# Performance work log

Hardware: AMD Instinct MI355X
Metric: run time of the kernel (lower is better)

## Reference

```python
import jax, jax.numpy as jnp
import numpy as np

H = 8  # num_heads


def setup_inputs() -> dict:
    key = jax.random.key(0)
    ks = jax.random.split(key, 10)
    B, N, C_sp, C_fd = 16, 4096, 768, 512
    s = 0.02
    return {
        "spatial_tokens": jax.random.normal(ks[0], (B, N, C_sp), jnp.float32),
        "freq_token": jax.random.normal(ks[1], (B, C_fd), jnp.float32),
        "Wq": jax.random.normal(ks[2], (C_sp, C_sp), jnp.float32) * s,
        "bq": jax.random.normal(ks[3], (C_sp,), jnp.float32) * s,
        "Wk": jax.random.normal(ks[4], (C_sp, C_fd), jnp.float32) * s,
        "bk": jax.random.normal(ks[5], (C_sp,), jnp.float32) * s,
        "Wv": jax.random.normal(ks[6], (C_sp, C_fd), jnp.float32) * s,
        "bv": jax.random.normal(ks[7], (C_sp,), jnp.float32) * s,
        "Wo": jax.random.normal(ks[8], (C_sp, C_sp), jnp.float32) * s,
        "bo": jax.random.normal(ks[9], (C_sp,), jnp.float32) * s,
    }


def reference(spatial_tokens, freq_token, Wq, bq, Wk, bk, Wv, bv, Wo, bo):
    B, N, C = spatial_tokens.shape
    D = C // H  # head_dim
    scale = jnp.sqrt(jnp.float32(D))
    # projections (torch Linear: x @ W.T + b)
    Q = spatial_tokens @ Wq.T + bq                 # [B, N, C]
    K = freq_token @ Wk.T + bk                     # [B, C] (single KV token)
    V = freq_token @ Wv.T + bv                     # [B, C]
    Qh = Q.reshape(B, N, H, D).transpose(0, 2, 1, 3)   # [B, H, N, D]
    Kh = K.reshape(B, 1, H, D).transpose(0, 2, 1, 3)   # [B, H, 1, D]
    Vh = V.reshape(B, 1, H, D).transpose(0, 2, 1, 3)   # [B, H, 1, D]
    scores = jnp.einsum('bhnd,bhkd->bhnk', Qh, Kh) / scale  # [B, H, N, 1]
    weights = jax.nn.softmax(scores, axis=-1)                # all-ones (k=1)
    attn = jnp.einsum('bhnk,bhkd->bhnd', weights, Vh)        # [B, H, N, D]
    attn = attn.transpose(0, 2, 1, 3).reshape(B, N, C)
    return attn @ Wo.T + bo                        # [B, N, C]
```

## Files before the change

kernel.cpp:

```cpp
#include <hip/hip_runtime.h>
#include <hip/hip_bf16.h>


#define B_   16
#define N_   4096
#define CSP  768
#define CFD  512

__global__ void __launch_bounds__(256) compute_v(const float* __restrict__ freq,
                                                 const float* __restrict__ Wv,
                                                 const float* __restrict__ bv,
                                                 float* __restrict__ V) {
    const int b = blockIdx.x;
    const int t = threadIdx.x;
    const int g = t >> 4;
    const int k = t & 15;
    const int j = blockIdx.y * 16 + g;

    const float4* wr = (const float4*)(Wv + (size_t)j * CFD);
    const float4* fr = (const float4*)(freq + (size_t)b * CFD);

    float acc = 0.f;
#pragma unroll
    for (int i = 0; i < CFD / 4 / 16; ++i) {
        float4 w = wr[k + 16 * i];
        float4 f = fr[k + 16 * i];
        acc += w.x * f.x + w.y * f.y + w.z * f.z + w.w * f.w;
    }
#pragma unroll
    for (int m = 8; m >= 1; m >>= 1)
        acc += __shfl_xor(acc, m);
    if (k == 0) V[(size_t)b * CSP + j] = acc + bv[j];
}

__global__ void __launch_bounds__(256) compute_o2(const float* __restrict__ V,
                                                  const float* __restrict__ Wo,
                                                  const float* __restrict__ bo,
                                                  float* __restrict__ O2) {
    const int b = blockIdx.x;
    const int t = threadIdx.x;
    const int g = t >> 4;
    const int k = t & 15;
    const int c = blockIdx.y * 16 + g;

    const float4* wr = (const float4*)(Wo + (size_t)c * CSP);
    const float4* vr = (const float4*)(V + (size_t)b * CSP);

    float acc = 0.f;
#pragma unroll
    for (int i = 0; i < CSP / 4 / 16; ++i) {
        float4 w = wr[k + 16 * i];
        float4 v = vr[k + 16 * i];
        acc += w.x * v.x + w.y * v.y + w.z * v.z + w.w * v.w;
    }
#pragma unroll
    for (int m = 8; m >= 1; m >>= 1)
        acc += __shfl_xor(acc, m);
    if (k == 0) O2[(size_t)b * CSP + c] = acc + bo[c];
}

__global__ void __launch_bounds__(192) broadcast_out(
    const float* __restrict__ O2,
    float* __restrict__ out)
{
    const int k  = blockIdx.x;
    const int b  = k >> 8;
    const int y0 = k & 255;
    const int t  = threadIdx.x;

    const float4 v = ((const float4*)(O2 + (size_t)b * CSP))[t];

    float4* dst = (float4*)(out + ((size_t)b * N_ + (size_t)y0) * CSP) + t;
#pragma unroll
    for (int i = 0; i < 16; ++i) {
        dst[(size_t)i * 256 * (CSP / 4)] = v;
    }
}

extern "C" void kernel_launch(void* const* d_in, const int* in_sizes, int n_in,
                              void* d_out, int out_size, void* d_ws, size_t ws_size,
                              hipStream_t stream) {
    const float* freq = (const float*)d_in[1];
    const float* Wv   = (const float*)d_in[6];
    const float* bv   = (const float*)d_in[7];
    const float* Wo   = (const float*)d_in[8];
    const float* bo   = (const float*)d_in[9];
    float* out = (float*)d_out;

    float* V  = (float*)d_ws;
    float* O2 = V + (size_t)B_ * CSP;

    compute_v <<<dim3(B_, CSP / 16), 256, 0, stream>>>(freq, Wv, bv, V);
    compute_o2<<<dim3(B_, CSP / 16), 256, 0, stream>>>(V, Wo, bo, O2);
    broadcast_out<<<dim3(4096), 192, 0, stream>>>(O2, out);
}
```

Measured before the change: 315.1 us.

## Fuse V and O2 projection kernels using per-batch atomic counter barrier

```diff
diff --git a/kernel.cpp b/kernel.cpp
--- a/kernel.cpp
+++ b/kernel.cpp
@@ -1,5 +1,4 @@
 #include <hip/hip_runtime.h>
-#include <hip/hip_bf16.h>
 
 
 #define B_   16
@@ -7,56 +6,66 @@
 #define CSP  768
 #define CFD  512
 
-__global__ void __launch_bounds__(256) compute_v(const float* __restrict__ freq,
-                                                 const float* __restrict__ Wv,
-                                                 const float* __restrict__ bv,
-                                                 float* __restrict__ V) {
+__global__ void __launch_bounds__(256) compute_vo2(
+    const float* __restrict__ freq,
+    const float* __restrict__ Wv,
+    const float* __restrict__ bv,
+    const float* __restrict__ Wo,
+    const float* __restrict__ bo,
+    float* __restrict__ V,
+    float* __restrict__ O2,
+    unsigned* __restrict__ cnt)
+{
     const int b = blockIdx.x;
     const int t = threadIdx.x;
     const int g = t >> 4;
     const int k = t & 15;
     const int j = blockIdx.y * 16 + g;
 
-    const float4* wr = (const float4*)(Wv + (size_t)j * CFD);
-    const float4* fr = (const float4*)(freq + (size_t)b * CFD);
+    {
+        const float4* wr = (const float4*)(Wv + (size_t)j * CFD);
+        const float4* fr = (const float4*)(freq + (size_t)b * CFD);
+        float acc = 0.f;
+#pragma unroll
+        for (int i = 0; i < CFD / 4 / 16; ++i) {
+            float4 w = wr[k + 16 * i];
+            float4 f = fr[k + 16 * i];
+            acc += w.x * f.x + w.y * f.y + w.z * f.z + w.w * f.w;
+        }
+#pragma unroll
+        for (int m = 8; m >= 1; m >>= 1)
+            acc += __shfl_xor(acc, m);
+        if (k == 0) V[(size_t)b * CSP + j] = acc + bv[j];
+    }
 
-    float acc = 0.f;
+    __syncthreads();
+    if (t == 0) {
+        __threadfence();
+        atomicAdd(&cnt[b], 1u);
+        while (__hip_atomic_load(&cnt[b], __ATOMIC_ACQUIRE,
+                                 __HIP_MEMORY_SCOPE_AGENT) < 48u) {
+            __builtin_amdgcn_s_sleep(1);
+        }
+        __threadfence();
+    }
+    __syncthreads();
+
+    {
+        const int c = j;
+        const float4* wr = (const float4*)(Wo + (size_t)c * CSP);
+        const float4* vr = (const float4*)(V + (size_t)b * CSP);
+        float acc = 0.f;
 #pragma unroll
-    for (int i = 0; i < CFD / 4 / 16; ++i) {
-        float4 w = wr[k + 16 * i];
-        float4 f = fr[k + 16 * i];
-        acc += w.x * f.x + w.y * f.y + w.z * f.z + w.w * f.w;
+        for (int i = 0; i < CSP / 4 / 16; ++i) {
+            float4 w = wr[k + 16 * i];
+            float4 v = vr[k + 16 * i];
+            acc += w.x * v.x + w.y * v.y + w.z * v.z + w.w * v.w;
+        }
+#pragma unroll
+        for (int m = 8; m >= 1; m >>= 1)
+            acc += __shfl_xor(acc, m);
+        if (k == 0) O2[(size_t)b * CSP + c] = acc + bo[c];
     }
-#pragma unroll
-    for (int m = 8; m >= 1; m >>= 1)
-        acc += __shfl_xor(acc, m);
-    if (k == 0) V[(size_t)b * CSP + j] = acc + bv[j];
-}
-
-__global__ void __launch_bounds__(256) compute_o2(const float* __restrict__ V,
-                                                  const float* __restrict__ Wo,
-                                                  const float* __restrict__ bo,
-                                                  float* __restrict__ O2) {
-    const int b = blockIdx.x;
-    const int t = threadIdx.x;
-    const int g = t >> 4;
-    const int k = t & 15;
-    const int c = blockIdx.y * 16 + g;
-
-    const float4* wr = (const float4*)(Wo + (size_t)c * CSP);
-    const float4* vr = (const float4*)(V + (size_t)b * CSP);
-
-    float acc = 0.f;
-#pragma unroll
-    for (int i = 0; i < CSP / 4 / 16; ++i) {
-        float4 w = wr[k + 16 * i];
-        float4 v = vr[k + 16 * i];
-        acc += w.x * v.x + w.y * v.y + w.z * v.z + w.w * v.w;
-    }
-#pragma unroll
-    for (int m = 8; m >= 1; m >>= 1)
-        acc += __shfl_xor(acc, m);
-    if (k == 0) O2[(size_t)b * CSP + c] = acc + bo[c];
 }
 
 __global__ void __launch_bounds__(192) broadcast_out(
@@ -89,8 +98,11 @@
 
     float* V  = (float*)d_ws;
     float* O2 = V + (size_t)B_ * CSP;
+    unsigned* cnt = (unsigned*)(O2 + (size_t)B_ * CSP);
 
-    compute_v <<<dim3(B_, CSP / 16), 256, 0, stream>>>(freq, Wv, bv, V);
-    compute_o2<<<dim3(B_, CSP / 16), 256, 0, stream>>>(V, Wo, bo, O2);
+    hipMemsetAsync(cnt, 0, B_ * sizeof(unsigned), stream);
+
+    compute_vo2<<<dim3(B_, CSP / 16), 256, 0, stream>>>(freq, Wv, bv, Wo, bo,
+                                                        V, O2, cnt);
     broadcast_out<<<dim3(4096), 192, 0, stream>>>(O2, out);
 }
```

After: 404.1 us. 28.3% more time.
